# Optimization experiments

Hardware: AMD Instinct MI355X
Metric: run time of the kernel (lower is better)

## Reference

```python
import jax, jax.numpy as jnp
import numpy as np
from jax import lax

K = 3       # kernel_size
G = 2       # group
STRIDE = 2
BN_EPS = 1e-5


def setup_inputs() -> dict:
    key = jax.random.key(0)
    k1, k2, k3, k4, k5, k6 = jax.random.split(key, 6)
    n, c, h, w = 16, 64, 128, 128
    gk2 = G * K * K
    x = jax.random.normal(k1, (n, c, h, w), dtype=jnp.float32)
    # kaiming_normal_(fan_out) std = sqrt(2 / (out_ch * k * k))
    std = float(np.sqrt(2.0 / (gk2 * K * K)))
    conv_w = jax.random.normal(k2, (gk2, c, K, K), dtype=jnp.float32) * std
    bn_gamma = jax.random.uniform(k3, (gk2,), dtype=jnp.float32, minval=0.5, maxval=1.5)
    bn_beta = jax.random.normal(k4, (gk2,), dtype=jnp.float32) * 0.1
    bn_mean = jax.random.normal(k5, (gk2,), dtype=jnp.float32) * 0.1
    bn_var = jax.random.uniform(k6, (gk2,), dtype=jnp.float32, minval=0.5, maxval=1.5)
    return {"x": x, "conv_w": conv_w, "bn_gamma": bn_gamma, "bn_beta": bn_beta,
            "bn_mean": bn_mean, "bn_var": bn_var}


def _pasa(x, conv_w, bn_gamma, bn_beta, bn_mean, bn_var):
    n, c, h, w = x.shape
    p = K // 2
    xp = jnp.pad(x, ((0, 0), (0, 0), (p, p), (p, p)), mode="reflect")
    # attention logits: conv over padded input, 'VALID' -> same h, w
    sigma = lax.conv_general_dilated(
        xp, conv_w, window_strides=(1, 1), padding="VALID",
        dimension_numbers=("NCHW", "OIHW", "NCHW"))
    # BatchNorm (inference) folded into scale/shift
    inv = bn_gamma * lax.rsqrt(bn_var + BN_EPS)
    sigma = sigma * inv[None, :, None, None] + (bn_beta - bn_mean * inv)[None, :, None, None]
    # softmax over the full g*k*k channel dim (as in the original Softmax(dim=1))
    sigma = jax.nn.softmax(sigma, axis=1)            # [n, g*k*k, h, w]
    sigma = sigma.reshape(n, G, K * K, h, w)
    # im2col: gather k*k shifted views of the padded input -> [n, c, k*k, h, w]
    patches = jnp.stack(
        [xp[:, :, i:i + h, j:j + w] for i in range(K) for j in range(K)], axis=2)
    patches = patches.reshape(n, G, c // G, K * K, h, w)
    # softmax-weighted aggregation over the kernel window
    out = jnp.einsum("ngckhw,ngkhw->ngchw", patches, sigma).reshape(n, c, h, w)
    return out[:, :, ::STRIDE, ::STRIDE]


def reference(x, conv_w, bn_gamma, bn_beta, bn_mean, bn_var):
    return _pasa(x, conv_w, bn_gamma, bn_beta, bn_mean, bn_var)
```

## Files before the change

kernel.cpp:

```cpp
#include <hip/hip_runtime.h>

#define N_  16
#define C_  64
#define H_  128
#define W_  128
#define HO_ 64
#define WO_ 64
#define CO_ 18

#define BK     584
#define BROWS  20
#define BBYTES_PAD 23424
#define NSHORT (BBYTES_PAD/2)
#define AOFF   BBYTES_PAD
#define SIGOFF (AOFF + 3*128*128)
#define LDSBYTES (SIGOFF + 64*21*4)
#define SHIFTOFF BBYTES_PAD

typedef _Float16 f16;
typedef f16 f16x4 __attribute__((ext_vector_type(4)));
typedef f16 f16x8 __attribute__((ext_vector_type(8)));
typedef float f4v  __attribute__((ext_vector_type(4)));

__global__ void pasa_prep(const float* __restrict__ cw,
                          const float* __restrict__ gamma,
                          const float* __restrict__ beta,
                          const float* __restrict__ mean,
                          const float* __restrict__ var,
                          float* __restrict__ ws)
{
    const int i = blockIdx.x * 256 + threadIdx.x;
    if (i < NSHORT) {
        const int o = i / BK, kk = i % BK;
        unsigned short bits = 0;
        if (o < CO_ && kk < 576) {
            const int tap = kk >> 6, c = kk & 63;
            const float inv = gamma[o] * rsqrtf(var[o] + 1e-5f);
            const f16 h = (f16)(cw[o*576 + c*9 + tap] * inv);
            bits = *(const unsigned short*)&h;
        }
        ((unsigned short*)ws)[i] = bits;
    }
    if (i < CO_) {
        const float inv = gamma[i] * rsqrtf(var[i] + 1e-5f);
        *(float*)((char*)ws + SHIFTOFF + i*4) = beta[i] - mean[i] * inv;
    }
}

__global__ __launch_bounds__(512)
void pasa_main(const float* __restrict__ x,
               const float* __restrict__ wt,
               float* __restrict__ out)
{
    __shared__ __align__(128) char lds[LDSBYTES];

    const int tid  = threadIdx.x;
    const int lane = tid & 63;
    const int bx = blockIdx.x;
    const int ho = ((bx & 7) << 3) | (bx >> 3);
    const int n  = blockIdx.y;

    int r0 = 2*ho - 1; if (r0 < 0) r0 = 1;
    const int r1 = 2*ho, r2 = 2*ho + 1;
    const float* __restrict__ xn = x + (size_t)n * (C_*H_*W_);

    {
        const unsigned* __restrict__ src = (const unsigned*)wt;
        unsigned* dst = (unsigned*)lds;
        for (int i = tid; i < BBYTES_PAD/4; i += 512) dst[i] = src[i];
    }
    if (tid < 384) {
        const int y    = tid >> 7;
        const int xcol = tid & 127;
        const int row  = (y == 0) ? r0 : (y == 1 ? r1 : r2);
        const float* __restrict__ bse = xn + row*W_ + xcol;
        char* cell = lds + AOFF + ((y*128 + xcol) << 7);
        const int sw = ((xcol >> 1) & 7) << 4;
        #pragma unroll
        for (int s = 0; s < 8; ++s) {
            f16x8 v;
            #pragma unroll
            for (int t = 0; t < 8; ++t)
                v[t] = (f16)bse[(8*s + t) * (H_*W_)];
            *(f16x8*)(cell + ((s*16) ^ sw)) = v;
        }
    }
    __syncthreads();

    const int wv = tid >> 6;
    const int mt = wv >> 1, nt = wv & 1;
    const int p  = lane & 15, lg = lane >> 4;

    int xcA[3], swA[3];
    #pragma unroll
    for (int kj = 0; kj < 3; ++kj) {
        int xc = 32*mt + 2*p + kj - 1; if (xc < 0) xc = 1;
        xcA[kj] = xc; swA[kj] = ((xc >> 1) & 7) << 4;
    }
    const int o    = nt*16 + p;
    const int oeff = (o < BROWS) ? o : 18;
    const char* __restrict__ brow = lds + oeff*(BK*2) + lg*8;

    f4v acc = {0.f, 0.f, 0.f, 0.f};
    #pragma unroll
    for (int ki = 0; ki < 3; ++ki) {
        #pragma unroll
        for (int kj = 0; kj < 3; ++kj) {
            const char* __restrict__ abase = lds + AOFF + ((ki*128 + xcA[kj]) << 7);
            const int sw = swA[kj];
            #pragma unroll
            for (int kc = 0; kc < 4; ++kc) {
                const f16x4 a = *(const f16x4*)(abase + ((kc*32 + lg*8) ^ sw));
                const f16x4 b = *(const f16x4*)(brow + (ki*3 + kj)*128 + kc*32);
                acc = __builtin_amdgcn_mfma_f32_16x16x16f16(a, b, acc, 0, 0, 0);
            }
        }
    }

    {
        float* sig_lds = (float*)(lds + SIGOFF);
        if (o < CO_) {
            #pragma unroll
            for (int r = 0; r < 4; ++r)
                sig_lds[(mt*16 + lg*4 + r)*21 + o] = acc[r];
        }
    }
    __syncthreads();

    const int wo = tid & 63;
    const int sp = tid >> 6;
    const float* __restrict__ shift = (const float*)((const char*)wt + SHIFTOFF);
    const float* sig_lds = (const float*)(lds + SIGOFF);

    float sig[CO_];
    float mx = -3.4e38f;
    #pragma unroll
    for (int oo = 0; oo < CO_; ++oo) {
        sig[oo] = sig_lds[wo*21 + oo] + shift[oo];
        mx = fmaxf(mx, sig[oo]);
    }
    float sum = 0.f;
    #pragma unroll
    for (int oo = 0; oo < CO_; ++oo) { sig[oo] = __expf(sig[oo] - mx); sum += sig[oo]; }
    const float rs = 1.f / sum;

    float pw[9];
    if ((sp >> 2) == 0) {
        #pragma unroll
        for (int k = 0; k < 9; ++k) pw[k] = sig[k] * rs;
    } else {
        #pragma unroll
        for (int k = 0; k < 9; ++k) pw[k] = sig[9 + k] * rs;
    }

    const int c1 = 2*wo;
    int c0 = c1 - 1; if (c0 < 0) c0 = 1;
    #pragma unroll
    for (int j = 0; j < 8; ++j) {
        const int c = sp * 8 + j;
        const float* __restrict__ xc = xn + c * (H_*W_);
        float a = xc[r0*W_ + c0] * pw[0];
        const float2 a12 = *(const float2*)(xc + r0*W_ + c1);
        a = fmaf(a12.x, pw[1], a);
        a = fmaf(a12.y, pw[2], a);
        a = fmaf(xc[r1*W_ + c0], pw[3], a);
        const float2 a45 = *(const float2*)(xc + r1*W_ + c1);
        a = fmaf(a45.x, pw[4], a);
        a = fmaf(a45.y, pw[5], a);
        a = fmaf(xc[r2*W_ + c0], pw[6], a);
        const float2 a78 = *(const float2*)(xc + r2*W_ + c1);
        a = fmaf(a78.x, pw[7], a);
        a = fmaf(a78.y, pw[8], a);
        out[(((size_t)n*C_ + c)*HO_ + ho)*WO_ + wo] = a;
    }
}

extern "C" void kernel_launch(void* const* d_in, const int* in_sizes, int n_in,
                              void* d_out, int out_size, void* d_ws, size_t ws_size,
                              hipStream_t stream) {
    const float* x     = (const float*)d_in[0];
    const float* cw    = (const float*)d_in[1];
    const float* gamma = (const float*)d_in[2];
    const float* beta  = (const float*)d_in[3];
    const float* mean  = (const float*)d_in[4];
    const float* var   = (const float*)d_in[5];
    float* out = (float*)d_out;
    float* ws  = (float*)d_ws;

    pasa_prep<<<(NSHORT + 255) / 256, 256, 0, stream>>>(cw, gamma, beta, mean, var, ws);
    dim3 grid(HO_, N_);
    pasa_main<<<grid, 512, 0, stream>>>(x, ws, out);
}
```

Baseline: 44.68 us.

## Load MFMA A-operands directly from global memory instead of staging in LDS

Removes the LDS staging of the three input rows as swizzled f16 tiles. Each lane now reads its conv A-fragments straight from global memory (scalar plus float2 loads, converted to f16), with the three kj taps fused into one load group per kc. This shrinks LDS from about 74KB to about 28KB and adds a launch-bounds occupancy hint, aiming for more resident blocks and less staging work. The cost is redundant, strided global/L2 reads across the two nt waves and lanes, and the MFMAs must wait on global load latency.

Result: slower. 48.26 us (+8.0%).

```diff
diff --git a/kernel.cpp b/kernel.cpp
--- a/kernel.cpp
+++ b/kernel.cpp
@@ -12,14 +12,12 @@
 #define BROWS  20
 #define BBYTES_PAD 23424
 #define NSHORT (BBYTES_PAD/2)
-#define AOFF   BBYTES_PAD
-#define SIGOFF (AOFF + 3*128*128)
-#define LDSBYTES (SIGOFF + 64*21*4)
 #define SHIFTOFF BBYTES_PAD
+#define SIGOFF  BBYTES_PAD
+#define LDSBYTES (BBYTES_PAD + 64*19*4)
 
 typedef _Float16 f16;
 typedef f16 f16x4 __attribute__((ext_vector_type(4)));
-typedef f16 f16x8 __attribute__((ext_vector_type(8)));
 typedef float f4v  __attribute__((ext_vector_type(4)));
 
 __global__ void pasa_prep(const float* __restrict__ cw,
@@ -47,12 +45,12 @@
     }
 }
 
-__global__ __launch_bounds__(512)
+__global__ __launch_bounds__(512, 8)
 void pasa_main(const float* __restrict__ x,
                const float* __restrict__ wt,
                float* __restrict__ out)
 {
-    __shared__ __align__(128) char lds[LDSBYTES];
+    __shared__ __align__(16) char lds[LDSBYTES];
 
     const int tid  = threadIdx.x;
     const int lane = tid & 63;
@@ -65,24 +63,12 @@
     const float* __restrict__ xn = x + (size_t)n * (C_*H_*W_);
 
     {
-        const unsigned* __restrict__ src = (const unsigned*)wt;
-        unsigned* dst = (unsigned*)lds;
-        for (int i = tid; i < BBYTES_PAD/4; i += 512) dst[i] = src[i];
-    }
-    if (tid < 384) {
-        const int y    = tid >> 7;
-        const int xcol = tid & 127;
-        const int row  = (y == 0) ? r0 : (y == 1 ? r1 : r2);
-        const float* __restrict__ bse = xn + row*W_ + xcol;
-        char* cell = lds + AOFF + ((y*128 + xcol) << 7);
-        const int sw = ((xcol >> 1) & 7) << 4;
+        const float4* __restrict__ src = (const float4*)wt;
+        float4* dst = (float4*)lds;
         #pragma unroll
-        for (int s = 0; s < 8; ++s) {
-            f16x8 v;
-            #pragma unroll
-            for (int t = 0; t < 8; ++t)
-                v[t] = (f16)bse[(8*s + t) * (H_*W_)];
-            *(f16x8*)(cell + ((s*16) ^ sw)) = v;
+        for (int it = 0; it < 3; ++it) {
+            const int i = tid + it*512;
+            if (i < BBYTES_PAD/16) dst[i] = src[i];
         }
     }
     __syncthreads();
@@ -90,30 +76,40 @@
     const int wv = tid >> 6;
     const int mt = wv >> 1, nt = wv & 1;
     const int p  = lane & 15, lg = lane >> 4;
+    const int pos = mt*16 + p;
 
-    int xcA[3], swA[3];
-    #pragma unroll
-    for (int kj = 0; kj < 3; ++kj) {
-        int xc = 32*mt + 2*p + kj - 1; if (xc < 0) xc = 1;
-        xcA[kj] = xc; swA[kj] = ((xc >> 1) & 7) << 4;
-    }
+    const int x0 = 2*pos;
+    int xm1 = x0 - 1; if (xm1 < 0) xm1 = 1;
+    const int rows[3] = {r0, r1, r2};
+
     const int o    = nt*16 + p;
-    const int oeff = (o < BROWS) ? o : 18;
-    const char* __restrict__ brow = lds + oeff*(BK*2) + lg*8;
+    const int oeff = (o < CO_) ? o : CO_;
+    const char* __restrict__ bb = lds + oeff*(BK*2) + lg*8;
 
     f4v acc = {0.f, 0.f, 0.f, 0.f};
     #pragma unroll
     for (int ki = 0; ki < 3; ++ki) {
+        const float* __restrict__ rp  = xn + rows[ki]*W_;
+        const float* __restrict__ am1 = rp + xm1;
+        const float* __restrict__ a01 = rp + x0;
         #pragma unroll
-        for (int kj = 0; kj < 3; ++kj) {
-            const char* __restrict__ abase = lds + AOFF + ((ki*128 + xcA[kj]) << 7);
-            const int sw = swA[kj];
+        for (int kc = 0; kc < 4; ++kc) {
+            const int cb = kc*16 + lg*4;
+            f16x4 f0, f1, f2;
             #pragma unroll
-            for (int kc = 0; kc < 4; ++kc) {
-                const f16x4 a = *(const f16x4*)(abase + ((kc*32 + lg*8) ^ sw));
-                const f16x4 b = *(const f16x4*)(brow + (ki*3 + kj)*128 + kc*32);
-                acc = __builtin_amdgcn_mfma_f32_16x16x16f16(a, b, acc, 0, 0, 0);
+            for (int i = 0; i < 4; ++i) {
+                const size_t co = (size_t)(cb + i) * (H_*W_);
+                f0[i] = (f16)am1[co];
+                const float2 t = *(const float2*)(a01 + co);
+                f1[i] = (f16)t.x;
+                f2[i] = (f16)t.y;
             }
+            const f16x4 b0 = *(const f16x4*)(bb + (ki*3+0)*128 + kc*32);
+            const f16x4 b1 = *(const f16x4*)(bb + (ki*3+1)*128 + kc*32);
+            const f16x4 b2 = *(const f16x4*)(bb + (ki*3+2)*128 + kc*32);
+            acc = __builtin_amdgcn_mfma_f32_16x16x16f16(f0, b0, acc, 0, 0, 0);
+            acc = __builtin_amdgcn_mfma_f32_16x16x16f16(f1, b1, acc, 0, 0, 0);
+            acc = __builtin_amdgcn_mfma_f32_16x16x16f16(f2, b2, acc, 0, 0, 0);
         }
     }
 
@@ -122,7 +118,7 @@
         if (o < CO_) {
             #pragma unroll
             for (int r = 0; r < 4; ++r)
-                sig_lds[(mt*16 + lg*4 + r)*21 + o] = acc[r];
+                sig_lds[(mt*16 + lg*4 + r)*19 + o] = acc[r];
         }
     }
     __syncthreads();
@@ -136,7 +132,7 @@
     float mx = -3.4e38f;
     #pragma unroll
     for (int oo = 0; oo < CO_; ++oo) {
-        sig[oo] = sig_lds[wo*21 + oo] + shift[oo];
+        sig[oo] = sig_lds[wo*19 + oo] + shift[oo];
         mx = fmaxf(mx, sig[oo]);
     }
     float sum = 0.f;
```
